# Kernel tuning notes

Measured on AMD Instinct MI355X. Metric: run time of the kernel, lower is better.

## Reference

```python
import jax, jax.numpy as jnp
import numpy as np

B, T = 2, 2048
V, C, H = 32000, 1024, 16
HS = C // H  # 64
W_SCALE = 0.02


def setup_inputs() -> dict:
    key = jax.random.key(0)
    ks = jax.random.split(key, 8)
    x = jax.random.randint(ks[0], (B, T), 0, V)
    tok_emb = jax.random.normal(ks[1], (V, C), jnp.float32) * W_SCALE
    pos_emb = jax.random.normal(ks[2], (T, C), jnp.float32) * W_SCALE
    wq = jax.random.normal(ks[3], (H, C, HS), jnp.float32) * W_SCALE
    wk = jax.random.normal(ks[4], (H, C, HS), jnp.float32) * W_SCALE
    wv = jax.random.normal(ks[5], (H, C, HS), jnp.float32) * W_SCALE
    bq = jnp.zeros((H, HS), jnp.float32)
    bk = jnp.zeros((H, HS), jnp.float32)
    bv = jnp.zeros((H, HS), jnp.float32)
    w_head = jax.random.normal(ks[6], (C, V), jnp.float32) * W_SCALE
    b_head = jnp.zeros((V,), jnp.float32)
    return dict(x=x, tok_emb=tok_emb, pos_emb=pos_emb, wq=wq, bq=bq,
                wk=wk, bk=bk, wv=wv, bv=bv, w_head=w_head, b_head=b_head)


def reference(x, tok_emb, pos_emb, wq, bq, wk, bk, wv, bv, w_head, b_head):
    Bx, Tx = x.shape
    Cx = tok_emb.shape[1]
    h = tok_emb[x] + pos_emb[:Tx]  # [B,T,C]
    # all heads batched: per-head Linear layers stacked on leading H axis
    q = jnp.einsum('btc,hcd->bhtd', h, wq) + bq[None, :, None, :]
    k = jnp.einsum('btc,hcd->bhtd', h, wk) + bk[None, :, None, :]
    v = jnp.einsum('btc,hcd->bhtd', h, wv) + bv[None, :, None, :]
    # NOTE: original scales by n_embd**-0.5 (full C), not head_size**-0.5
    att = jnp.einsum('bhtd,bhsd->bhts', q, k) * (Cx ** -0.5)
    causal = jnp.tril(jnp.ones((Tx, Tx), dtype=bool))
    att = jnp.where(causal, att, jnp.finfo(att.dtype).min)
    att = jax.nn.softmax(att, axis=-1)
    y = jnp.einsum('bhts,bhsd->bhtd', att, v)  # [B,H,T,HS]
    y = jnp.transpose(y, (0, 2, 1, 3)).reshape(Bx, Tx, Cx)  # concat heads
    logits = jnp.einsum('btc,cv->btv', y, w_head) + b_head  # [B,T,V]
    return logits
```

## Files before the change

kernel.cpp:

```cpp
#include <hip/hip_runtime.h>

#define T_SEQ 2048
#define C_DIM 1024
#define H_N   16
#define HS_D  64
#define V_DIM 32000

typedef float f32x4 __attribute__((ext_vector_type(4)));
typedef __bf16 bf16x8 __attribute__((ext_vector_type(8)));
typedef unsigned short us4 __attribute__((ext_vector_type(4)));
typedef unsigned short us8 __attribute__((ext_vector_type(8)));

__device__ inline unsigned short f2bf(float f) {
  unsigned int u = __float_as_uint(f);
  u = (u + 0x7FFFu + ((u >> 16) & 1u)) >> 16;
  return (unsigned short)u;
}

__global__ __launch_bounds__(256) void embed_kernel(
    const int* __restrict__ x, const float* __restrict__ tok,
    const float* __restrict__ pos, unsigned short* __restrict__ h) {
  int idx = blockIdx.x * 256 + threadIdx.x;
  int bt = idx >> 8;
  int c4 = (idx & 255) * 4;
  int t = bt & (T_SEQ - 1);
  int tokid = x[bt];
  f32x4 a = *(const f32x4*)(tok + (size_t)tokid * C_DIM + c4);
  f32x4 b = *(const f32x4*)(pos + (size_t)t * C_DIM + c4);
  f32x4 s = a + b;
  us4 o;
  o[0] = f2bf(s[0]); o[1] = f2bf(s[1]); o[2] = f2bf(s[2]); o[3] = f2bf(s[3]);
  *(us4*)(h + (size_t)bt * C_DIM + c4) = o;
}

__global__ __launch_bounds__(256) void repack_qkv(
    const float* __restrict__ wq, const float* __restrict__ wk, const float* __restrict__ wv,
    const float* __restrict__ bq, const float* __restrict__ bk, const float* __restrict__ bv,
    unsigned short* __restrict__ wt, float* __restrict__ biasp) {
  int which = blockIdx.y;
  const float* w = (which == 0) ? wq : (which == 1) ? wk : wv;
  int i = blockIdx.x * 256 + threadIdx.x;
  int d = i & 63;
  int c = (i >> 6) & (C_DIM - 1);
  int hh = i >> 16;
  int n = which * 1024 + hh * 64 + d;
  wt[(size_t)n * C_DIM + c] = f2bf(w[i]);
  if (c == 0) {
    const float* bb = (which == 0) ? bq : (which == 1) ? bk : bv;
    biasp[n] = bb[hh * 64 + d];
  }
}

__global__ __launch_bounds__(256) void repack_whead(
    const float* __restrict__ wh, unsigned short* __restrict__ wht) {
  __shared__ float tile[64][65];
  int v0 = blockIdx.x * 64;
  int c0 = blockIdx.y * 64;
  int tr = threadIdx.x >> 6;
  int tc = threadIdx.x & 63;
#pragma unroll
  for (int i = 0; i < 16; ++i) {
    int r = i * 4 + tr;
    tile[r][tc] = wh[(size_t)(c0 + r) * V_DIM + v0 + tc];
  }
  __syncthreads();
#pragma unroll
  for (int i = 0; i < 16; ++i) {
    int vr = i * 4 + tr;
    wht[(size_t)(v0 + vr) * C_DIM + c0 + tc] = f2bf(tile[tc][vr]);
  }
}

__global__ __launch_bounds__(256) void gemm_bf16_o16(
    const unsigned short* __restrict__ A, const unsigned short* __restrict__ Bt,
    const float* __restrict__ bias, unsigned short* __restrict__ Cout, int N, int Mtiles) {
  const int K = 1024;
  __shared__ unsigned short As[128 * 32];
  __shared__ unsigned short Bs[128 * 32];
  int tid = threadIdx.x;
  int lane = tid & 63, wvi = tid >> 6;
  int cpx = gridDim.x >> 3;
  int lin = blockIdx.x;
  int wg = (lin & 7) * cpx + (lin >> 3);
  int m0 = (wg % Mtiles) * 128;
  int n0 = (wg / Mtiles) * 128;
  int wmm = (wvi >> 1) * 64, wnn = (wvi & 1) * 64;
  int r16 = lane & 15, gg = lane >> 4;
  f32x4 acc[4][4] = {};

  for (int k0 = 0; k0 < K; k0 += 32) {
#pragma unroll
    for (int it = 0; it < 2; ++it) {
      int ch = it * 256 + wvi * 64 + lane;
      int row = ch >> 2, cc = (ch & 3) * 8;
      const unsigned short* ga = A + (size_t)(m0 + row) * K + k0 + cc;
      __builtin_amdgcn_global_load_lds(
          (const __attribute__((address_space(1))) void*)ga,
          (__attribute__((address_space(3))) void*)&As[ch * 8], 16, 0, 0);
      const unsigned short* gb = Bt + (size_t)(n0 + row) * K + k0 + cc;
      __builtin_amdgcn_global_load_lds(
          (const __attribute__((address_space(1))) void*)gb,
          (__attribute__((address_space(3))) void*)&Bs[ch * 8], 16, 0, 0);
    }
    __syncthreads();
    bf16x8 fa[4], fb[4];
#pragma unroll
    for (int m = 0; m < 4; ++m)
      fa[m] = *(const bf16x8*)&As[(wmm + m * 16 + r16) * 32 + gg * 8];
#pragma unroll
    for (int n = 0; n < 4; ++n)
      fb[n] = *(const bf16x8*)&Bs[(wnn + n * 16 + r16) * 32 + gg * 8];
#pragma unroll
    for (int m = 0; m < 4; ++m)
#pragma unroll
      for (int n = 0; n < 4; ++n)
        acc[m][n] = __builtin_amdgcn_mfma_f32_16x16x32_bf16(fa[m], fb[n], acc[m][n], 0, 0, 0);
    __syncthreads();
  }
#pragma unroll
  for (int m = 0; m < 4; ++m) {
    int row = m0 + wmm + m * 16 + gg * 4;
#pragma unroll
    for (int n = 0; n < 4; ++n) {
      int col = n0 + wnn + n * 16 + r16;
      float bval = bias[col];
#pragma unroll
      for (int j = 0; j < 4; ++j)
        Cout[(size_t)(row + j) * N + col] = f2bf(acc[m][n][j] + bval);
    }
  }
}

__global__ __launch_bounds__(256) void transpose_v(
    const unsigned short* __restrict__ qkv, unsigned short* __restrict__ vt) {
  __shared__ unsigned short tile[64][72];
  int bh = blockIdx.y;
  int b = bh >> 4, h = bh & 15;
  int tb = blockIdx.x;
  int r = threadIdx.x >> 2;
  int c0 = (threadIdx.x & 3) * 16;
  const unsigned short* src = qkv + ((size_t)(b * T_SEQ) + tb * 64 + r) * 3072 + 2048 + h * 64 + c0;
  *(us8*)&tile[r][c0] = *(const us8*)src;
  *(us8*)&tile[r][c0 + 8] = *(const us8*)(src + 8);
  __syncthreads();
  unsigned short* dst = vt + (size_t)bh * 64 * T_SEQ + (size_t)r * T_SEQ + tb * 64 + c0;
  us8 o1, o2;
#pragma unroll
  for (int i = 0; i < 8; ++i) { o1[i] = tile[c0 + i][r]; o2[i] = tile[c0 + 8 + i][r]; }
  *(us8*)dst = o1;
  *(us8*)(dst + 8) = o2;
}

#define GK 1024
#define GNT 16

__global__ __launch_bounds__(512, 1) void gemm256(
    const unsigned short* __restrict__ A, const unsigned short* __restrict__ Bt,
    const float* __restrict__ bias, float* __restrict__ Cout, int N, int Mtiles) {
  __shared__ unsigned short As[2][256 * 64];
  __shared__ unsigned short Bs[2][256 * 64];
  int tid = threadIdx.x;
  int lane = tid & 63;
  int wid = tid >> 6;
  int wm = wid >> 2, wn = wid & 3;
  int l16 = lane & 15, g = lane >> 4;
  int swz = l16 & 7;

  int cpx = gridDim.x >> 3;
  int lin = blockIdx.x;
  int wg = (lin & 7) * cpx + (lin >> 3);
  int m0 = (wg % Mtiles) * 256;
  int n0 = (wg / Mtiles) * 256;

  auto stageA2 = [&](int kt, int mh) {
    unsigned short* lds = As[kt & 1];
#pragma unroll
    for (int q = 0; q < 2; ++q) {
      int chunk = q * 512 + tid;
      int rr = chunk >> 3;
      int row = (rr & 63) + ((rr >> 6) << 7) + mh * 64;
      int cpos = chunk & 7;
      int c = cpos ^ (row & 7);
      const unsigned short* src = A + (size_t)(m0 + row) * GK + kt * 64 + c * 8;
      __builtin_amdgcn_global_load_lds(
          (const __attribute__((address_space(1))) void*)src,
          (__attribute__((address_space(3))) void*)(lds + row * 64 + cpos * 8), 16, 0, 0);
    }
  };
  auto stageB4 = [&](int kt) {
    unsigned short* lds = Bs[kt & 1];
#pragma unroll
    for (int q = 0; q < 4; ++q) {
      int chunk = q * 512 + tid;
      int row = chunk >> 3;
      int cpos = chunk & 7;
      int c = cpos ^ (row & 7);
      const unsigned short* src = Bt + (size_t)(n0 + row) * GK + kt * 64 + c * 8;
      __builtin_amdgcn_global_load_lds(
          (const __attribute__((address_space(1))) void*)src,
          (__attribute__((address_space(3))) void*)(lds + row * 64 + cpos * 8), 16, 0, 0);
    }
  };

  stageA2(0, 0); stageB4(0);
  stageA2(0, 1);
  stageA2(1, 0); stageB4(1);
  asm volatile("s_waitcnt vmcnt(8)" ::: "memory");
  asm volatile("s_barrier" ::: "memory");

  f32x4 acc[8][4] = {};

  for (int t = 0; t < GNT; ++t) {
    const char* Ab = (const char*)As[t & 1];
    const char* Bb = (const char*)Bs[t & 1];
    bf16x8 bA[4][2], bB[4][2];

#pragma unroll
    for (int mi = 0; mi < 4; ++mi) {
      int row = wm * 128 + mi * 16 + l16;
#pragma unroll
      for (int kk = 0; kk < 2; ++kk)
        bA[mi][kk] = *(const bf16x8*)(Ab + row * 128 + (((kk * 4 + g) ^ swz) * 16));
    }
#pragma unroll
    for (int ni = 0; ni < 4; ++ni) {
      int row = wn * 64 + ni * 16 + l16;
#pragma unroll
      for (int kk = 0; kk < 2; ++kk)
        bB[ni][kk] = *(const bf16x8*)(Bb + row * 128 + (((kk * 4 + g) ^ swz) * 16));
    }
    if (t + 1 < GNT) stageA2(t + 1, 1);
    asm volatile("s_barrier" ::: "memory");
    asm volatile("s_waitcnt lgkmcnt(0)" ::: "memory");
    __builtin_amdgcn_sched_barrier(0);
    __builtin_amdgcn_s_setprio(1);
#pragma unroll
    for (int mi = 0; mi < 4; ++mi)
#pragma unroll
      for (int ni = 0; ni < 4; ++ni)
#pragma unroll
        for (int kk = 0; kk < 2; ++kk)
          acc[mi][ni] = __builtin_amdgcn_mfma_f32_16x16x32_bf16(bA[mi][kk], bB[ni][kk], acc[mi][ni], 0, 0, 0);
    __builtin_amdgcn_s_setprio(0);
    if (t + 1 < GNT) asm volatile("s_waitcnt vmcnt(8)" ::: "memory");
    else             asm volatile("s_waitcnt vmcnt(0)" ::: "memory");
    asm volatile("s_barrier" ::: "memory");

#pragma unroll
    for (int mi = 0; mi < 4; ++mi) {
      int row = wm * 128 + 64 + mi * 16 + l16;
#pragma unroll
      for (int kk = 0; kk < 2; ++kk)
        bA[mi][kk] = *(const bf16x8*)(Ab + row * 128 + (((kk * 4 + g) ^ swz) * 16));
    }
    if (t + 2 < GNT) { stageA2(t + 2, 0); stageB4(t + 2); }
    asm volatile("s_barrier" ::: "memory");
    asm volatile("s_waitcnt lgkmcnt(0)" ::: "memory");
    __builtin_amdgcn_sched_barrier(0);
    __builtin_amdgcn_s_setprio(1);
#pragma unroll
    for (int mi = 0; mi < 4; ++mi)
#pragma unroll
      for (int ni = 0; ni < 4; ++ni)
#pragma unroll
        for (int kk = 0; kk < 2; ++kk)
          acc[4 + mi][ni] = __builtin_amdgcn_mfma_f32_16x16x32_bf16(bA[mi][kk], bB[ni][kk], acc[4 + mi][ni], 0, 0, 0);
    __builtin_amdgcn_s_setprio(0);
    if (t + 2 < GNT)       asm volatile("s_waitcnt vmcnt(8)" ::: "memory");
    else if (t + 2 == GNT) asm volatile("s_waitcnt vmcnt(2)" ::: "memory");
    asm volatile("s_barrier" ::: "memory");
  }

#pragma unroll
  for (int mf = 0; mf < 8; ++mf) {
    int row = m0 + wm * 128 + mf * 16 + g * 4;
#pragma unroll
    for (int n = 0; n < 4; ++n) {
      int col = n0 + wn * 64 + n * 16 + l16;
      float bv = bias[col];
#pragma unroll
      for (int j = 0; j < 4; ++j)
        __builtin_nontemporal_store(acc[mf][n][j] + bv, &Cout[(size_t)(row + j) * N + col]);
    }
  }
}

__global__ __launch_bounds__(256) void attn_mfma(
    const unsigned short* __restrict__ qkv, const unsigned short* __restrict__ vt,
    unsigned short* __restrict__ y) {
  __shared__ unsigned short Kl[2][4096];
  __shared__ unsigned short Vl[2][4096];
  __shared__ char Pl[8192];

  int bh = blockIdx.y;
  int b = bh >> 4, h = bh & 15;
  int qb = (T_SEQ / 64 - 1) - blockIdx.x;
  int tid = threadIdx.x;
  int lane = tid & 63, w = tid >> 6;
  int l16 = lane & 15, g = lane >> 4;
  size_t bT = (size_t)b * T_SEQ;
  const float scale2 = 0.03125f * 1.44269504f;

  const unsigned short* qrow = qkv + (bT + qb * 64 + w * 16 + l16) * 3072 + h * 64;
  bf16x8 qf[2] = { *(const bf16x8*)(qrow + g * 8), *(const bf16x8*)(qrow + 32 + g * 8) };

  f32x4 yacc[4] = {};
  float mrun[4], lrun[4];
#pragma unroll
  for (int j = 0; j < 4; ++j) { mrun[j] = -3.0e38f; lrun[j] = 0.f; }

  auto stageK = [&](int kb, int buf) {
    const unsigned short* base = qkv + (bT + kb * 64) * 3072 + 1024 + h * 64;
#pragma unroll
    for (int q2 = 0; q2 < 2; ++q2) {
      int chunk = q2 * 256 + tid;
      int row = chunk >> 3, cpos = chunk & 7;
      int c = cpos ^ (row & 7);
      const unsigned short* src = base + (size_t)row * 3072 + c * 8;
      __builtin_amdgcn_global_load_lds(
          (const __attribute__((address_space(1))) void*)src,
          (__attribute__((address_space(3))) void*)&Kl[buf][chunk * 8], 16, 0, 0);
    }
  };
  auto stageV = [&](int kb, int buf) {
    const unsigned short* base = vt + (size_t)bh * 64 * T_SEQ + kb * 64;
#pragma unroll
    for (int q2 = 0; q2 < 2; ++q2) {
      int chunk = q2 * 256 + tid;
      int row = chunk >> 3, cpos = chunk & 7;
      int c = cpos ^ (row & 7);
      const unsigned short* src = base + (size_t)row * T_SEQ + c * 8;
      __builtin_amdgcn_global_load_lds(
          (const __attribute__((address_space(1))) void*)src,
          (__attribute__((address_space(3))) void*)&Vl[buf][chunk * 8], 16, 0, 0);
    }
  };

  stageK(0, 0); stageV(0, 0);

  for (int kb = 0; kb <= qb; ++kb) {
    int buf = kb & 1;
    if (kb < qb) { stageK(kb + 1, buf ^ 1); stageV(kb + 1, buf ^ 1); }
    if (kb < qb) asm volatile("s_waitcnt vmcnt(4)" ::: "memory");
    else         asm volatile("s_waitcnt vmcnt(0)" ::: "memory");
    asm volatile("s_barrier" ::: "memory");

    f32x4 s[4] = {};
#pragma unroll
    for (int kk = 0; kk < 2; ++kk)
#pragma unroll
      for (int n = 0; n < 4; ++n) {
        int krow = n * 16 + l16;
        bf16x8 fb = *(const bf16x8*)((const char*)Kl[buf] + krow * 128 + (((kk * 4 + g) ^ (krow & 7)) * 16));
        s[n] = __builtin_amdgcn_mfma_f32_16x16x32_bf16(qf[kk], fb, s[n], 0, 0, 0);
      }

    bool diag = (kb == qb);
    float pr[4][4];
    float corr[4];
#pragma unroll
    for (int j = 0; j < 4; ++j) {
      int rloc = w * 16 + g * 4 + j;
      float m = -3.0e38f;
#pragma unroll
      for (int n = 0; n < 4; ++n) {
        float v = s[n][j] * scale2;
        if (diag && (n * 16 + l16) > rloc) v = -3.0e38f;
        pr[n][j] = v;
        m = fmaxf(m, v);
      }
      m = fmaxf(m, __shfl_xor(m, 1));
      m = fmaxf(m, __shfl_xor(m, 2));
      m = fmaxf(m, __shfl_xor(m, 4));
      m = fmaxf(m, __shfl_xor(m, 8));
      float mn = fmaxf(mrun[j], m);
      corr[j] = exp2f(mrun[j] - mn);
      mrun[j] = mn;
      float ps = 0.f;
#pragma unroll
      for (int n = 0; n < 4; ++n) {
        float e = exp2f(pr[n][j] - mn);
        pr[n][j] = e;
        ps += e;
      }
      ps += __shfl_xor(ps, 1);
      ps += __shfl_xor(ps, 2);
      ps += __shfl_xor(ps, 4);
      ps += __shfl_xor(ps, 8);
      lrun[j] = lrun[j] * corr[j] + ps;
    }
#pragma unroll
    for (int n = 0; n < 4; ++n)
#pragma unroll
      for (int j = 0; j < 4; ++j)
        yacc[n][j] *= corr[j];

#pragma unroll
    for (int j = 0; j < 4; ++j) {
      int row = w * 16 + g * 4 + j;
#pragma unroll
      for (int n = 0; n < 4; ++n)
        *(unsigned short*)(Pl + ((row * 128 + (n * 16 + l16) * 2) ^ ((row & 7) << 4))) = f2bf(pr[n][j]);
    }

#pragma unroll
    for (int kk = 0; kk < 2; ++kk) {
      int prow = w * 16 + l16;
      bf16x8 fa = *(const bf16x8*)(Pl + ((prow * 128 + (kk * 32 + g * 8) * 2) ^ ((prow & 7) << 4)));
#pragma unroll
      for (int n = 0; n < 4; ++n) {
        int vrow = n * 16 + l16;
        bf16x8 fbv = *(const bf16x8*)((const char*)Vl[buf] + vrow * 128 + (((kk * 4 + g) ^ (vrow & 7)) * 16));
        yacc[n] = __builtin_amdgcn_mfma_f32_16x16x32_bf16(fa, fbv, yacc[n], 0, 0, 0);
      }
    }
    asm volatile("s_barrier" ::: "memory");
  }

#pragma unroll
  for (int j = 0; j < 4; ++j) {
    float inv = 1.0f / lrun[j];
    int row = qb * 64 + w * 16 + g * 4 + j;
    unsigned short* yo = y + (bT + row) * C_DIM + h * 64;
#pragma unroll
    for (int n = 0; n < 4; ++n)
      yo[n * 16 + l16] = f2bf(yacc[n][j] * inv);
  }
}

extern "C" void kernel_launch(void* const* d_in, const int* in_sizes, int n_in,
                              void* d_out, int out_size, void* d_ws, size_t ws_size,
                              hipStream_t stream) {
  const int*   x    = (const int*)d_in[0];
  const float* tok  = (const float*)d_in[1];
  const float* pos  = (const float*)d_in[2];
  const float* wq   = (const float*)d_in[3];
  const float* bq   = (const float*)d_in[4];
  const float* wk   = (const float*)d_in[5];
  const float* bk   = (const float*)d_in[6];
  const float* wv   = (const float*)d_in[7];
  const float* bv   = (const float*)d_in[8];
  const float* wh   = (const float*)d_in[9];
  const float* bhd  = (const float*)d_in[10];
  float* out = (float*)d_out;

  char* ws = (char*)d_ws;
  size_t off = 0;
  auto alloc = [&](size_t bytes) {
    void* p = ws + off;
    off += (bytes + 255) & ~(size_t)255;
    return p;
  };
  unsigned short* h_bf    = (unsigned short*)alloc((size_t)4096 * 1024 * 2);
  unsigned short* wqkv_t  = (unsigned short*)alloc((size_t)3072 * 1024 * 2);
  float*          qbias   = (float*)alloc((size_t)3072 * 4);
  unsigned short* wh_t    = (unsigned short*)alloc((size_t)V_DIM * 1024 * 2);
  unsigned short* qkv_bf  = (unsigned short*)alloc((size_t)4096 * 3072 * 2);
  unsigned short* vtb     = (unsigned short*)alloc((size_t)32 * 64 * T_SEQ * 2);
  unsigned short* ybf     = (unsigned short*)alloc((size_t)4096 * 1024 * 2);

  embed_kernel<<<4096, 256, 0, stream>>>(x, tok, pos, h_bf);
  repack_qkv<<<dim3(4096, 3), 256, 0, stream>>>(wq, wk, wv, bq, bk, bv, wqkv_t, qbias);
  repack_whead<<<dim3(V_DIM / 64, 16), 256, 0, stream>>>(wh, wh_t);
  gemm_bf16_o16<<<768, 256, 0, stream>>>(h_bf, wqkv_t, qbias, qkv_bf, 3072, 32);
  transpose_v<<<dim3(T_SEQ / 64, 2 * H_N), 256, 0, stream>>>(qkv_bf, vtb);
  attn_mfma<<<dim3(T_SEQ / 64, 2 * H_N), 256, 0, stream>>>(qkv_bf, vtb, ybf);
  gemm256<<<2000, 512, 0, stream>>>(ybf, wh_t, bhd, out, V_DIM, 16);
}
```

Before: 559.8 us.

## Replace 256x256 head GEMM with simpler 128x128 double-buffered tile kernel

Replaces the 512-thread 256x256-tile LM-head GEMM, with its split-A half-tile pipelining, by a 256-thread 128x128-tile kernel. The new kernel uses plain double buffering that waits on all loads before each step, and stores output with regular instead of nontemporal stores. Smaller tiles give more blocks and occupancy per CU. In exchange, each tile reuses less data, so global and LDS traffic per FLOP rises, and the full vmcnt(0) wait leaves less load/compute overlap.

New measurement: 731.5 us. 1.31x slower.

```diff
diff --git a/kernel.cpp b/kernel.cpp
--- a/kernel.cpp
+++ b/kernel.cpp
@@ -154,83 +154,68 @@
 #define GK 1024
 #define GNT 16
 
-__global__ __launch_bounds__(512, 1) void gemm256(
+__global__ __launch_bounds__(256) void gemm128d(
     const unsigned short* __restrict__ A, const unsigned short* __restrict__ Bt,
     const float* __restrict__ bias, float* __restrict__ Cout, int N, int Mtiles) {
-  __shared__ unsigned short As[2][256 * 64];
-  __shared__ unsigned short Bs[2][256 * 64];
+  __shared__ unsigned short As[2][128 * 64];
+  __shared__ unsigned short Bs[2][128 * 64];
   int tid = threadIdx.x;
   int lane = tid & 63;
   int wid = tid >> 6;
-  int wm = wid >> 2, wn = wid & 3;
+  int wm = wid >> 1, wn = wid & 1;
   int l16 = lane & 15, g = lane >> 4;
-  int swz = l16 & 7;
 
   int cpx = gridDim.x >> 3;
   int lin = blockIdx.x;
   int wg = (lin & 7) * cpx + (lin >> 3);
-  int m0 = (wg % Mtiles) * 256;
-  int n0 = (wg / Mtiles) * 256;
-
-  auto stageA2 = [&](int kt, int mh) {
-    unsigned short* lds = As[kt & 1];
-#pragma unroll
-    for (int q = 0; q < 2; ++q) {
-      int chunk = q * 512 + tid;
-      int rr = chunk >> 3;
-      int row = (rr & 63) + ((rr >> 6) << 7) + mh * 64;
+  int m0 = (wg % Mtiles) * 128;
+  int n0 = (wg / Mtiles) * 128;
+
+  auto stage = [&](const unsigned short* __restrict__ G, int base,
+                   unsigned short* lds, int kt) {
+#pragma unroll
+    for (int q = 0; q < 4; ++q) {
+      int chunk = q * 256 + tid;
+      int row = chunk >> 3;
       int cpos = chunk & 7;
       int c = cpos ^ (row & 7);
-      const unsigned short* src = A + (size_t)(m0 + row) * GK + kt * 64 + c * 8;
+      const unsigned short* src = G + (size_t)(base + row) * GK + kt * 64 + c * 8;
       __builtin_amdgcn_global_load_lds(
           (const __attribute__((address_space(1))) void*)src,
           (__attribute__((address_space(3))) void*)(lds + row * 64 + cpos * 8), 16, 0, 0);
     }
   };
-  auto stageB4 = [&](int kt) {
-    unsigned short* lds = Bs[kt & 1];
-#pragma unroll
-    for (int q = 0; q < 4; ++q) {
-      int chunk = q * 512 + tid;
-      int row = chunk >> 3;
-      int cpos = chunk & 7;
-      int c = cpos ^ (row & 7);
-      const unsigned short* src = Bt + (size_t)(n0 + row) * GK + kt * 64 + c * 8;
-      __builtin_amdgcn_global_load_lds(
-          (const __attribute__((address_space(1))) void*)src,
-          (__attribute__((address_space(3))) void*)(lds + row * 64 + cpos * 8), 16, 0, 0);
-    }
-  };
-
-  stageA2(0, 0); stageB4(0);
-  stageA2(0, 1);
-  stageA2(1, 0); stageB4(1);
-  asm volatile("s_waitcnt vmcnt(8)" ::: "memory");
-  asm volatile("s_barrier" ::: "memory");
-
-  f32x4 acc[8][4] = {};
+
+  stage(A, m0, As[0], 0);
+  stage(Bt, n0, Bs[0], 0);
+
+  f32x4 acc[4][4] = {};
 
   for (int t = 0; t < GNT; ++t) {
-    const char* Ab = (const char*)As[t & 1];
-    const char* Bb = (const char*)Bs[t & 1];
+    int buf = t & 1;
+    asm volatile("s_waitcnt vmcnt(0)" ::: "memory");
+    asm volatile("s_barrier" ::: "memory");
+    if (t + 1 < GNT) {
+      stage(A, m0, As[buf ^ 1], t + 1);
+      stage(Bt, n0, Bs[buf ^ 1], t + 1);
+    }
+    const char* Ab = (const char*)As[buf];
+    const char* Bb = (const char*)Bs[buf];
     bf16x8 bA[4][2], bB[4][2];
-
 #pragma unroll
     for (int mi = 0; mi < 4; ++mi) {
-      int row = wm * 128 + mi * 16 + l16;
+      int row = wm * 64 + mi * 16 + l16;
 #pragma unroll
       for (int kk = 0; kk < 2; ++kk)
-        bA[mi][kk] = *(const bf16x8*)(Ab + row * 128 + (((kk * 4 + g) ^ swz) * 16));
+        bA[mi][kk] = *(const bf16x8*)(Ab + row * 128 + (((kk * 4 + g) ^ (row & 7)) * 16));
     }
 #pragma unroll
     for (int ni = 0; ni < 4; ++ni) {
       int row = wn * 64 + ni * 16 + l16;
 #pragma unroll
       for (int kk = 0; kk < 2; ++kk)
-        bB[ni][kk] = *(const bf16x8*)(Bb + row * 128 + (((kk * 4 + g) ^ swz) * 16));
-    }
-    if (t + 1 < GNT) stageA2(t + 1, 1);
-    asm volatile("s_barrier" ::: "memory");
+        bB[ni][kk] = *(const bf16x8*)(Bb + row * 128 + (((kk * 4 + g) ^ (row & 7)) * 16));
+    }
     asm volatile("s_waitcnt lgkmcnt(0)" ::: "memory");
     __builtin_amdgcn_sched_barrier(0);
     __builtin_amdgcn_s_setprio(1);
@@ -242,45 +227,18 @@
         for (int kk = 0; kk < 2; ++kk)
           acc[mi][ni] = __builtin_amdgcn_mfma_f32_16x16x32_bf16(bA[mi][kk], bB[ni][kk], acc[mi][ni], 0, 0, 0);
     __builtin_amdgcn_s_setprio(0);
-    if (t + 1 < GNT) asm volatile("s_waitcnt vmcnt(8)" ::: "memory");
-    else             asm volatile("s_waitcnt vmcnt(0)" ::: "memory");
-    asm volatile("s_barrier" ::: "memory");
-
-#pragma unroll
-    for (int mi = 0; mi < 4; ++mi) {
-      int row = wm * 128 + 64 + mi * 16 + l16;
-#pragma unroll
-      for (int kk = 0; kk < 2; ++kk)
-        bA[mi][kk] = *(const bf16x8*)(Ab + row * 128 + (((kk * 4 + g) ^ swz) * 16));
-    }
-    if (t + 2 < GNT) { stageA2(t + 2, 0); stageB4(t + 2); }
-    asm volatile("s_barrier" ::: "memory");
-    asm volatile("s_waitcnt lgkmcnt(0)" ::: "memory");
-    __builtin_amdgcn_sched_barrier(0);
-    __builtin_amdgcn_s_setprio(1);
-#pragma unroll
-    for (int mi = 0; mi < 4; ++mi)
-#pragma unroll
-      for (int ni = 0; ni < 4; ++ni)
-#pragma unroll
-        for (int kk = 0; kk < 2; ++kk)
-          acc[4 + mi][ni] = __builtin_amdgcn_mfma_f32_16x16x32_bf16(bA[mi][kk], bB[ni][kk], acc[4 + mi][ni], 0, 0, 0);
-    __builtin_amdgcn_s_setprio(0);
-    if (t + 2 < GNT)       asm volatile("s_waitcnt vmcnt(8)" ::: "memory");
-    else if (t + 2 == GNT) asm volatile("s_waitcnt vmcnt(2)" ::: "memory");
-    asm volatile("s_barrier" ::: "memory");
-  }
-
-#pragma unroll
-  for (int mf = 0; mf < 8; ++mf) {
-    int row = m0 + wm * 128 + mf * 16 + g * 4;
-#pragma unroll
-    for (int n = 0; n < 4; ++n) {
-      int col = n0 + wn * 64 + n * 16 + l16;
+  }
+
+#pragma unroll
+  for (int mi = 0; mi < 4; ++mi) {
+    int row = m0 + wm * 64 + mi * 16 + g * 4;
+#pragma unroll
+    for (int ni = 0; ni < 4; ++ni) {
+      int col = n0 + wn * 64 + ni * 16 + l16;
       float bv = bias[col];
 #pragma unroll
       for (int j = 0; j < 4; ++j)
-        __builtin_nontemporal_store(acc[mf][n][j] + bv, &Cout[(size_t)(row + j) * N + col]);
+        Cout[(size_t)(row + j) * N + col] = acc[mi][ni][j] + bv;
     }
   }
 }
@@ -465,5 +423,5 @@
   gemm_bf16_o16<<<768, 256, 0, stream>>>(h_bf, wqkv_t, qbias, qkv_bf, 3072, 32);
   transpose_v<<<dim3(T_SEQ / 64, 2 * H_N), 256, 0, stream>>>(qkv_bf, vtb);
   attn_mfma<<<dim3(T_SEQ / 64, 2 * H_N), 256, 0, stream>>>(qkv_bf, vtb, ybf);
-  gemm256<<<2000, 512, 0, stream>>>(ybf, wh_t, bhd, out, V_DIM, 16);
-}
+  gemm128d<<<8000, 256, 0, stream>>>(ybf, wh_t, bhd, out, V_DIM, 32);
+}
```
